# Optimization experiments

Measured on AMD Instinct MI355X. Metric: run time of the kernel, lower is better.

The kernel has to match this reference:

```python
import jax, jax.numpy as jnp
import numpy as np

N, QLEN, KLEN = 4, 2048, 2048
QDIM = KVDIM = 512
EMBED, HEADS = 1024, 16
HEAD_DIM = EMBED // HEADS


def setup_inputs() -> dict:
    key = jax.random.key(0)
    ks = jax.random.split(key, 7)
    return {
        "queries": jax.random.normal(ks[0], (N, QLEN, QDIM), dtype=jnp.float32),
        "keys": jax.random.normal(ks[1], (1, KLEN, KVDIM), dtype=jnp.float32),
        "values": jax.random.normal(ks[2], (1, KLEN, KVDIM), dtype=jnp.float32),
        "mask": jax.random.randint(ks[3], (N, 1, 1, KLEN), 0, 2, dtype=jnp.int32),
        "Wq": jax.random.normal(ks[4], (QDIM, EMBED), dtype=jnp.float32) * (QDIM ** -0.5),
        "Wk": jax.random.normal(ks[5], (KVDIM, EMBED), dtype=jnp.float32) * (KVDIM ** -0.5),
        "Wv": jax.random.normal(ks[6], (KVDIM, EMBED), dtype=jnp.float32) * (KVDIM ** -0.5),
    }


def reference(queries, keys, values, mask, Wq, Wk, Wv):
    # Projections (Linear, no bias)
    q = (queries @ Wq).reshape(N, QLEN, HEADS, HEAD_DIM)      # [N, Q, H, D]
    k = (keys @ Wk).reshape(KLEN, HEADS, HEAD_DIM)            # [K, H, D] (batch-1, shared)
    v = (values @ Wv).reshape(KLEN, HEADS, HEAD_DIM)          # [K, H, D]

    # energy: [N, H, Q, K]
    energy = jnp.einsum('nqhd,khd->nhqk', q, k)
    energy = jnp.where(mask == 0, jnp.float32(-1e20), energy)
    attn = jax.nn.softmax(energy / jnp.float32(HEAD_DIM ** 0.5), axis=3)

    out = jnp.einsum('nhqk,khd->nqhd', attn, v)               # [N, Q, H, D]
    return out.reshape(N, QLEN, EMBED)
```

## Files before the change

kernel.cpp:

```cpp
#include <hip/hip_runtime.h>

#define NB 4
#define QLEN 2048
#define KLEN 2048
#define QDIM 512
#define EMBED 1024
#define HEADS 16
#define HD 64

typedef __bf16 bf16x8 __attribute__((ext_vector_type(8)));
typedef float f32x2 __attribute__((ext_vector_type(2)));
typedef float f32x4 __attribute__((ext_vector_type(4)));
typedef float f32x16 __attribute__((ext_vector_type(16)));

#define CLOG 0.18033688011112042f

__device__ __forceinline__ float fexp2(float x) {
#if __has_builtin(__builtin_amdgcn_exp2f)
    return __builtin_amdgcn_exp2f(x);
#else
    float r;
    asm("v_exp_f32 %0, %1\n\ts_nop 1" : "=v"(r) : "v"(x));
    return r;
#endif
}

#if __has_builtin(__builtin_amdgcn_sched_barrier)
#define SCHED_FENCE() __builtin_amdgcn_sched_barrier(0)
#else
#define SCHED_FENCE()
#endif

__device__ __forceinline__ void dma16(const void* g, void* l) {
    __builtin_amdgcn_global_load_lds(
        (const __attribute__((address_space(1))) void*)g,
        (__attribute__((address_space(3))) void*)l, 16, 0, 0);
}

__global__ __launch_bounds__(256) void prep(const float* __restrict__ q,
                                            const float* __restrict__ k,
                                            const float* __restrict__ v,
                                            const float* __restrict__ Wq,
                                            const float* __restrict__ Wk,
                                            const float* __restrict__ Wv,
                                            __bf16* __restrict__ qd,
                                            __bf16* __restrict__ kd,
                                            __bf16* __restrict__ vd,
                                            __bf16* __restrict__ WtQ,
                                            __bf16* __restrict__ WtK,
                                            __bf16* __restrict__ WtV) {
    __shared__ float tile[32][33];
    int b = blockIdx.x, tid = threadIdx.x;
    if (b < 3072) {
        const float* src; __bf16* dst; int cb;
        if (b < 2048)      { src = q; dst = qd; cb = b; }
        else if (b < 2560) { src = k; dst = kd; cb = b - 2048; }
        else               { src = v; dst = vd; cb = b - 2560; }
        int i = (cb * 256 + tid) * 8;
        float4 a0 = *(const float4*)&src[i];
        float4 a1 = *(const float4*)&src[i + 4];
        bf16x8 o;
        o[0] = (__bf16)a0.x; o[1] = (__bf16)a0.y; o[2] = (__bf16)a0.z; o[3] = (__bf16)a0.w;
        o[4] = (__bf16)a1.x; o[5] = (__bf16)a1.y; o[6] = (__bf16)a1.z; o[7] = (__bf16)a1.w;
        *(bf16x8*)&dst[i] = o;
    } else {
        int tb = b - 3072;
        int which = tb >> 9, r = tb & 511;
        const float* src = (which == 0) ? Wq : (which == 1) ? Wk : Wv;
        __bf16* dst = (which == 0) ? WtQ : (which == 1) ? WtK : WtV;
        float scale = (which == 0) ? CLOG : 1.0f;
        int e0 = (r & 31) * 32, c0 = (r >> 5) * 32;
        int tx = tid & 31, ty = tid >> 5;
        for (int i = 0; i < 4; i++)
            tile[ty + 8 * i][tx] = src[(c0 + ty + 8 * i) * EMBED + e0 + tx];
        __syncthreads();
        for (int i = 0; i < 4; i++)
            dst[(e0 + ty + 8 * i) * QDIM + c0 + tx] = (__bf16)(tile[tx][ty + 8 * i] * scale);
    }
}

__device__ __forceinline__ void gemm_compute(const __bf16* As, const __bf16* Bs,
                                             int wr, int wc, int r16, int qq,
                                             f32x4 (&acc)[4][4]) {
    bf16x8 af[4], bq[4];
#pragma unroll
    for (int i = 0; i < 4; i++)
        af[i] = *(const bf16x8*)&As[(wr * 64 + i * 16 + r16) * 32 + qq * 8];
#pragma unroll
    for (int j = 0; j < 4; j++)
        bq[j] = *(const bf16x8*)&Bs[(wc * 64 + j * 16 + r16) * 32 + qq * 8];
#pragma unroll
    for (int i = 0; i < 4; i++)
#pragma unroll
        for (int j = 0; j < 4; j++)
            acc[i][j] = __builtin_amdgcn_mfma_f32_16x16x32_bf16(af[i], bq[j], acc[i][j], 0, 0, 0);
}

__device__ __forceinline__ void gemm128(const __bf16* __restrict__ A,
                                        const __bf16* __restrict__ Bt,
                                        __bf16* As0, __bf16* As1,
                                        __bf16* Bs0, __bf16* Bs1,
                                        int row0, int col0, f32x4 (&acc)[4][4]) {
    int tid = threadIdx.x, wave = tid >> 6, lane = tid & 63;
    int r16 = lane & 15, qq = lane >> 4;
    int wr = wave >> 1, wc = wave & 1;
    const __bf16* agp1 = A + (size_t)(row0 + (tid >> 2)) * QDIM + (tid & 3) * 8;
    const __bf16* agp2 = A + (size_t)(row0 + 64 + (tid >> 2)) * QDIM + (tid & 3) * 8;
    const __bf16* bgp1 = Bt + (size_t)(col0 + (tid >> 2)) * QDIM + (tid & 3) * 8;
    const __bf16* bgp2 = Bt + (size_t)(col0 + 64 + (tid >> 2)) * QDIM + (tid & 3) * 8;
    __bf16 *a0a = &As0[wave * 512], *a0b = &As0[2048 + wave * 512];
    __bf16 *a1a = &As1[wave * 512], *a1b = &As1[2048 + wave * 512];
    __bf16 *b0a = &Bs0[wave * 512], *b0b = &Bs0[2048 + wave * 512];
    __bf16 *b1a = &Bs1[wave * 512], *b1b = &Bs1[2048 + wave * 512];

    dma16(agp1, a0a); dma16(agp2, a0b);
    dma16(bgp1, b0a); dma16(bgp2, b0b);
    agp1 += 32; agp2 += 32; bgp1 += 32; bgp2 += 32;
    __syncthreads();

    for (int t = 0; t < 16; t += 2) {
        dma16(agp1, a1a); dma16(agp2, a1b);
        dma16(bgp1, b1a); dma16(bgp2, b1b);
        agp1 += 32; agp2 += 32; bgp1 += 32; bgp2 += 32;
        SCHED_FENCE();
        gemm_compute(As0, Bs0, wr, wc, r16, qq, acc);
        __syncthreads();
        if (t + 2 < 16) {
            dma16(agp1, a0a); dma16(agp2, a0b);
            dma16(bgp1, b0a); dma16(bgp2, b0b);
            agp1 += 32; agp2 += 32; bgp1 += 32; bgp2 += 32;
        }
        SCHED_FENCE();
        gemm_compute(As1, Bs1, wr, wc, r16, qq, acc);
        __syncthreads();
    }
}

__global__ __launch_bounds__(256) void proj_all(const __bf16* __restrict__ qin,
                                                const __bf16* __restrict__ kin,
                                                const __bf16* __restrict__ vin,
                                                const __bf16* __restrict__ wtq,
                                                const __bf16* __restrict__ wtk,
                                                const __bf16* __restrict__ wtv,
                                                __bf16* __restrict__ qout,
                                                __bf16* __restrict__ kout,
                                                __bf16* __restrict__ vtout) {
    __shared__ __align__(16) __bf16 As[2][128 * 32];
    __shared__ __align__(16) __bf16 Bs[2][128 * 32];
    int bid = blockIdx.x;
    const __bf16 *A, *Bt;
    int mode, b;
    if (bid < 512)      { A = qin; Bt = wtq; mode = 0; b = bid; }
    else if (bid < 640) { A = kin; Bt = wtk; mode = 1; b = bid - 512; }
    else                { A = wtv; Bt = vin; mode = 2; b = bid - 640; }
    int row0, col0;
    if (mode == 2) { row0 = (b >> 4) * 128; col0 = (b & 15) * 128; }
    else           { row0 = (b >> 3) * 128; col0 = (b & 7) * 128; }
    f32x4 acc[4][4] = {};
    gemm128(A, Bt, As[0], As[1], Bs[0], Bs[1], row0, col0, acc);
    int lane = threadIdx.x & 63, wave = threadIdx.x >> 6;
    int r16 = lane & 15, qq = lane >> 4;
    int wr = wave >> 1, wc = wave & 1;
#pragma unroll
    for (int i = 0; i < 4; i++)
#pragma unroll
        for (int j = 0; j < 4; j++)
#pragma unroll
            for (int rr = 0; rr < 4; rr++) {
                int grow = row0 + wr * 64 + i * 16 + qq * 4 + rr;
                int gcol = col0 + wc * 64 + j * 16 + r16;
                __bf16 v = (__bf16)acc[i][j][rr];
                if (mode == 0) {
                    int hh = gcol >> 6, d = gcol & 63;
                    int n = grow >> 11, qr = grow & 2047;
                    qout[((size_t)(n * HEADS + hh) * QLEN + qr) * HD + d] = v;
                } else if (mode == 1) {
                    int hh = gcol >> 6, d = gcol & 63;
                    kout[((size_t)hh * KLEN + grow) * HD + d] = v;
                } else {
                    vtout[(size_t)grow * KLEN + gcol] = v;
                }
            }
}

__device__ __forceinline__ void attn_tile(const __bf16* ksb, const __bf16* vsb,
                                          const float* mrow, const bf16x8 (&qfrag)[4],
                                          int col, int h,
                                          f32x16& o0, f32x16& o1, f32x2& rsl) {
    bf16x8 pfrag[4];
#pragma unroll
    for (int kt2 = 0; kt2 < 2; kt2++) {
        int R = kt2 * 32 + col;
        union { f32x16 v; f32x4 q[4]; } su;
#pragma unroll
        for (int G = 0; G < 4; G++)
            su.q[G] = *(const f32x4*)&mrow[kt2 * 32 + 16 * (G >> 1) + 8 * h + 4 * (G & 1)];
        f32x16 s = su.v;
        __builtin_amdgcn_s_setprio(1);
#pragma unroll
        for (int c = 0; c < 4; c++) {
            int cc = (2 * c + h) ^ (R & 7);
            bf16x8 kf = *(const bf16x8*)&ksb[(R * 8 + cc) * 8];
            s = __builtin_amdgcn_mfma_f32_32x32x16_bf16(kf, qfrag[c], s, 0, 0, 0);
        }
        __builtin_amdgcn_s_setprio(0);
#pragma unroll
        for (int G = 0; G < 4; G++) {
            int ci = 2 * kt2 + (G >> 1), e0 = (G & 1) * 4;
#pragma unroll
            for (int rr = 0; rr < 4; rr += 2) {
                float p0 = fexp2(s[4 * G + rr]);
                float p1 = fexp2(s[4 * G + rr + 1]);
                f32x2 pp; pp[0] = p0; pp[1] = p1;
                rsl += pp;
                pfrag[ci][e0 + rr] = (__bf16)p0;
                pfrag[ci][e0 + rr + 1] = (__bf16)p1;
            }
        }
    }
    __builtin_amdgcn_s_setprio(1);
#pragma unroll
    for (int c = 0; c < 4; c++) {
        int cc = (2 * c + h) ^ (col & 7);
        bf16x8 v0 = *(const bf16x8*)&vsb[(col * 8 + cc) * 8];
        bf16x8 v1 = *(const bf16x8*)&vsb[((32 + col) * 8 + cc) * 8];
        o0 = __builtin_amdgcn_mfma_f32_32x32x16_bf16(v0, pfrag[c], o0, 0, 0, 0);
        o1 = __builtin_amdgcn_mfma_f32_32x32x16_bf16(v1, pfrag[c], o1, 0, 0, 0);
    }
    __builtin_amdgcn_s_setprio(0);
}

__global__ __launch_bounds__(256, 4) void attn_kernel(const __bf16* __restrict__ qb,
                                                      const __bf16* __restrict__ kb,
                                                      const __bf16* __restrict__ vtb,
                                                      const int* __restrict__ mask,
                                                      float* __restrict__ out) {
    __shared__ __align__(16) __bf16 ks[2][4096];
    __shared__ __align__(16) __bf16 vs[2][4096];
    __shared__ __align__(16) float msf[KLEN];

    int tid = threadIdx.x, wave = tid >> 6, lane = tid & 63;
    int col = lane & 31, h = lane >> 5;
    int q0 = blockIdx.x * 128, hh = blockIdx.y, n = blockIdx.z;
    const __bf16* qg = qb + ((size_t)(n * HEADS + hh) * QLEN + q0 + wave * 32 + col) * HD;
    const __bf16* kg = kb + (size_t)hh * KLEN * HD;
    const __bf16* vg = vtb + (size_t)hh * HD * KLEN;
    const int* mg = mask + n * KLEN;

    bf16x8 qfrag[4];
#pragma unroll
    for (int c = 0; c < 4; c++) qfrag[c] = *(const bf16x8*)&qg[c * 16 + h * 8];

    int s1 = tid, R1 = s1 >> 3, c1 = (s1 & 7) ^ (R1 & 7);
    int s2 = tid + 256, R2 = s2 >> 3, c2 = (s2 & 7) ^ (R2 & 7);
    int g1 = (R1 & 0x33) | ((R1 & 4) << 1) | ((R1 & 8) >> 1);
    int g2 = (R2 & 0x33) | ((R2 & 4) << 1) | ((R2 & 8) >> 1);
    const __bf16* kgp1 = kg + g1 * HD + c1 * 8;
    const __bf16* kgp2 = kg + g2 * HD + c2 * 8;
    const __bf16* vgp1 = vg + (size_t)R1 * KLEN + c1 * 8;
    const __bf16* vgp2 = vg + (size_t)R2 * KLEN + c2 * 8;
    __bf16 *kl0a = &ks[0][wave * 512], *kl0b = &ks[0][2048 + wave * 512];
    __bf16 *kl1a = &ks[1][wave * 512], *kl1b = &ks[1][2048 + wave * 512];
    __bf16 *vl0a = &vs[0][wave * 512], *vl0b = &vs[0][2048 + wave * 512];
    __bf16 *vl1a = &vs[1][wave * 512], *vl1b = &vs[1][2048 + wave * 512];

    dma16(kgp1, kl0a); dma16(kgp2, kl0b);
    dma16(vgp1, vl0a); dma16(vgp2, vl0b);
    kgp1 += 64 * HD; kgp2 += 64 * HD; vgp1 += 64; vgp2 += 64;
    {
        int i8 = tid * 8;
        int4 ma = *(const int4*)&mg[i8];
        int4 mb = *(const int4*)&mg[i8 + 4];
        f32x4 fa, fb;
        fa[0] = ma.x ? 0.f : -1e30f; fa[1] = ma.y ? 0.f : -1e30f;
        fa[2] = ma.z ? 0.f : -1e30f; fa[3] = ma.w ? 0.f : -1e30f;
        fb[0] = mb.x ? 0.f : -1e30f; fb[1] = mb.y ? 0.f : -1e30f;
        fb[2] = mb.z ? 0.f : -1e30f; fb[3] = mb.w ? 0.f : -1e30f;
        *(f32x4*)&msf[i8] = fa;
        *(f32x4*)&msf[i8 + 4] = fb;
    }
    __syncthreads();

    f32x16 o0 = {}, o1 = {};
    f32x2 rsl = {};

    for (int t = 0; t < 32; t += 2) {
        dma16(kgp1, kl1a); dma16(kgp2, kl1b);
        dma16(vgp1, vl1a); dma16(vgp2, vl1b);
        kgp1 += 64 * HD; kgp2 += 64 * HD; vgp1 += 64; vgp2 += 64;
        SCHED_FENCE();
        attn_tile(ks[0], vs[0], &msf[t * 64], qfrag, col, h, o0, o1, rsl);
        __syncthreads();
        if (t + 2 < 32) {
            dma16(kgp1, kl0a); dma16(kgp2, kl0b);
            dma16(vgp1, vl0a); dma16(vgp2, vl0b);
            kgp1 += 64 * HD; kgp2 += 64 * HD; vgp1 += 64; vgp2 += 64;
        }
        SCHED_FENCE();
        attn_tile(ks[1], vs[1], &msf[(t + 1) * 64], qfrag, col, h, o0, o1, rsl);
        __syncthreads();
    }

    float rs = rsl[0] + rsl[1];
    rs += __shfl_xor(rs, 32);
    float inv = 1.0f / rs;
    float* op = out + ((size_t)n * QLEN + q0 + wave * 32 + col) * EMBED + hh * HD;
#pragma unroll
    for (int G = 0; G < 4; G++) {
        float4 t0, t1;
        t0.x = o0[4 * G + 0] * inv; t0.y = o0[4 * G + 1] * inv;
        t0.z = o0[4 * G + 2] * inv; t0.w = o0[4 * G + 3] * inv;
        t1.x = o1[4 * G + 0] * inv; t1.y = o1[4 * G + 1] * inv;
        t1.z = o1[4 * G + 2] * inv; t1.w = o1[4 * G + 3] * inv;
        *(float4*)&op[8 * G + 4 * h] = t0;
        *(float4*)&op[32 + 8 * G + 4 * h] = t1;
    }
}

extern "C" void kernel_launch(void* const* d_in, const int* in_sizes, int n_in,
                              void* d_out, int out_size, void* d_ws, size_t ws_size,
                              hipStream_t stream) {
    const float* queries = (const float*)d_in[0];
    const float* keys    = (const float*)d_in[1];
    const float* values  = (const float*)d_in[2];
    const int*   mask    = (const int*)d_in[3];
    const float* Wq      = (const float*)d_in[4];
    const float* Wk      = (const float*)d_in[5];
    const float* Wv      = (const float*)d_in[6];
    float* out = (float*)d_out;

    const size_t MiB = 1048576;
    char* ws = (char*)d_ws;
    __bf16* qbf   = (__bf16*)(ws);
    __bf16* kbf   = (__bf16*)(ws + 16 * MiB);
    __bf16* vtbf  = (__bf16*)(ws + 20 * MiB);
    __bf16* wtq   = (__bf16*)(ws + 24 * MiB);
    __bf16* wtk   = (__bf16*)(ws + 25 * MiB);
    __bf16* wtv   = (__bf16*)(ws + 26 * MiB);
    __bf16* qin   = (__bf16*)(ws + 27 * MiB);
    __bf16* kin   = (__bf16*)(ws + 35 * MiB);
    __bf16* vin   = (__bf16*)(ws + 37 * MiB);

    prep<<<4608, 256, 0, stream>>>(queries, keys, values, Wq, Wk, Wv,
                                   qin, kin, vin, wtq, wtk, wtv);
    proj_all<<<768, 256, 0, stream>>>(qin, kin, vin, wtq, wtk, wtv, qbf, kbf, vtbf);
    attn_kernel<<<dim3(QLEN / 128, HEADS, NB), 256, 0, stream>>>(qbf, kbf, vtbf, mask, out);
}
```

Baseline: 184.1 us.

## Read K/V tiles directly from global memory instead of LDS double-buffering

Removes the shared-memory staging of K and V tiles (async DMA into double-buffered LDS with swizzle and per-tile barriers). Each wave now loads its MFMA fragments straight from global memory, relying on L1/L2 caching since all waves of a block read the same K/V data. This drops the barriers and LDS traffic, and cuts LDS use, which can raise occupancy. The cost is redundant global/cache loads per wave and load latency that is no longer hidden by prefetch, leaving the MFMAs exposed to memory stalls.

```diff
diff --git a/kernel.cpp b/kernel.cpp
--- a/kernel.cpp
+++ b/kernel.cpp
@@ -183,14 +183,14 @@
             }
 }
 
-__device__ __forceinline__ void attn_tile(const __bf16* ksb, const __bf16* vsb,
+__device__ __forceinline__ void attn_tile(const __bf16* kt, const __bf16* vt,
                                           const float* mrow, const bf16x8 (&qfrag)[4],
-                                          int col, int h,
+                                          int col, int colp, int h,
                                           f32x16& o0, f32x16& o1, f32x2& rsl) {
     bf16x8 pfrag[4];
 #pragma unroll
     for (int kt2 = 0; kt2 < 2; kt2++) {
-        int R = kt2 * 32 + col;
+        const __bf16* kr = kt + (kt2 * 32 + colp) * HD + h * 8;
         union { f32x16 v; f32x4 q[4]; } su;
 #pragma unroll
         for (int G = 0; G < 4; G++)
@@ -199,8 +199,7 @@
         __builtin_amdgcn_s_setprio(1);
 #pragma unroll
         for (int c = 0; c < 4; c++) {
-            int cc = (2 * c + h) ^ (R & 7);
-            bf16x8 kf = *(const bf16x8*)&ksb[(R * 8 + cc) * 8];
+            bf16x8 kf = *(const bf16x8*)&kr[c * 16];
             s = __builtin_amdgcn_mfma_f32_32x32x16_bf16(kf, qfrag[c], s, 0, 0, 0);
         }
         __builtin_amdgcn_s_setprio(0);
@@ -218,12 +217,13 @@
             }
         }
     }
+    const __bf16* vr0 = vt + (size_t)col * KLEN + h * 8;
+    const __bf16* vr1 = vt + (size_t)(32 + col) * KLEN + h * 8;
     __builtin_amdgcn_s_setprio(1);
 #pragma unroll
     for (int c = 0; c < 4; c++) {
-        int cc = (2 * c + h) ^ (col & 7);
-        bf16x8 v0 = *(const bf16x8*)&vsb[(col * 8 + cc) * 8];
-        bf16x8 v1 = *(const bf16x8*)&vsb[((32 + col) * 8 + cc) * 8];
+        bf16x8 v0 = *(const bf16x8*)&vr0[c * 16];
+        bf16x8 v1 = *(const bf16x8*)&vr1[c * 16];
         o0 = __builtin_amdgcn_mfma_f32_32x32x16_bf16(v0, pfrag[c], o0, 0, 0, 0);
         o1 = __builtin_amdgcn_mfma_f32_32x32x16_bf16(v1, pfrag[c], o1, 0, 0, 0);
     }
@@ -235,12 +235,11 @@
                                                       const __bf16* __restrict__ vtb,
                                                       const int* __restrict__ mask,
                                                       float* __restrict__ out) {
-    __shared__ __align__(16) __bf16 ks[2][4096];
-    __shared__ __align__(16) __bf16 vs[2][4096];
     __shared__ __align__(16) float msf[KLEN];
 
     int tid = threadIdx.x, wave = tid >> 6, lane = tid & 63;
     int col = lane & 31, h = lane >> 5;
+    int colp = (col & 0x33) | ((col & 4) << 1) | ((col & 8) >> 1);
     int q0 = blockIdx.x * 128, hh = blockIdx.y, n = blockIdx.z;
     const __bf16* qg = qb + ((size_t)(n * HEADS + hh) * QLEN + q0 + wave * 32 + col) * HD;
     const __bf16* kg = kb + (size_t)hh * KLEN * HD;
@@ -251,22 +250,6 @@
 #pragma unroll
     for (int c = 0; c < 4; c++) qfrag[c] = *(const bf16x8*)&qg[c * 16 + h * 8];
 
-    int s1 = tid, R1 = s1 >> 3, c1 = (s1 & 7) ^ (R1 & 7);
-    int s2 = tid + 256, R2 = s2 >> 3, c2 = (s2 & 7) ^ (R2 & 7);
-    int g1 = (R1 & 0x33) | ((R1 & 4) << 1) | ((R1 & 8) >> 1);
-    int g2 = (R2 & 0x33) | ((R2 & 4) << 1) | ((R2 & 8) >> 1);
-    const __bf16* kgp1 = kg + g1 * HD + c1 * 8;
-    const __bf16* kgp2 = kg + g2 * HD + c2 * 8;
-    const __bf16* vgp1 = vg + (size_t)R1 * KLEN + c1 * 8;
-    const __bf16* vgp2 = vg + (size_t)R2 * KLEN + c2 * 8;
-    __bf16 *kl0a = &ks[0][wave * 512], *kl0b = &ks[0][2048 + wave * 512];
-    __bf16 *kl1a = &ks[1][wave * 512], *kl1b = &ks[1][2048 + wave * 512];
-    __bf16 *vl0a = &vs[0][wave * 512], *vl0b = &vs[0][2048 + wave * 512];
-    __bf16 *vl1a = &vs[1][wave * 512], *vl1b = &vs[1][2048 + wave * 512];
-
-    dma16(kgp1, kl0a); dma16(kgp2, kl0b);
-    dma16(vgp1, vl0a); dma16(vgp2, vl0b);
-    kgp1 += 64 * HD; kgp2 += 64 * HD; vgp1 += 64; vgp2 += 64;
     {
         int i8 = tid * 8;
         int4 ma = *(const int4*)&mg[i8];
@@ -284,22 +267,9 @@
     f32x16 o0 = {}, o1 = {};
     f32x2 rsl = {};
 
-    for (int t = 0; t < 32; t += 2) {
-        dma16(kgp1, kl1a); dma16(kgp2, kl1b);
-        dma16(vgp1, vl1a); dma16(vgp2, vl1b);
-        kgp1 += 64 * HD; kgp2 += 64 * HD; vgp1 += 64; vgp2 += 64;
-        SCHED_FENCE();
-        attn_tile(ks[0], vs[0], &msf[t * 64], qfrag, col, h, o0, o1, rsl);
-        __syncthreads();
-        if (t + 2 < 32) {
-            dma16(kgp1, kl0a); dma16(kgp2, kl0b);
-            dma16(vgp1, vl0a); dma16(vgp2, vl0b);
-            kgp1 += 64 * HD; kgp2 += 64 * HD; vgp1 += 64; vgp2 += 64;
-        }
-        SCHED_FENCE();
-        attn_tile(ks[1], vs[1], &msf[(t + 1) * 64], qfrag, col, h, o0, o1, rsl);
-        __syncthreads();
-    }
+    for (int t = 0; t < 32; ++t)
+        attn_tile(kg + (size_t)t * 64 * HD, vg + t * 64, &msf[t * 64],
+                  qfrag, col, colp, h, o0, o1, rsl);
 
     float rs = rsl[0] + rsl[1];
     rs += __shfl_xor(rs, 32);
```

New measurement: 344.2 us. +87.0%, slower.

## Double attention block to 8 waves covering 256 queries sharing K/V tiles

Applied to the files above, without the earlier changes.

The attention kernel now launches 512 threads per block, each block handling 256 query rows instead of 128, and half as many blocks. Each thread issues one K and one V async copy per tile rather than two, so every K/V tile loaded into shared memory serves twice as many waves. This halves global K/V traffic and per-thread load work, at the cost of larger blocks, fewer blocks in the grid (512), and more waves stalling at each block-wide barrier.

```diff
diff --git a/kernel.cpp b/kernel.cpp
--- a/kernel.cpp
+++ b/kernel.cpp
@@ -230,7 +230,7 @@
     __builtin_amdgcn_s_setprio(0);
 }
 
-__global__ __launch_bounds__(256, 4) void attn_kernel(const __bf16* __restrict__ qb,
+__global__ __launch_bounds__(512, 4) void attn_kernel(const __bf16* __restrict__ qb,
                                                       const __bf16* __restrict__ kb,
                                                       const __bf16* __restrict__ vtb,
                                                       const int* __restrict__ mask,
@@ -241,7 +241,7 @@
 
     int tid = threadIdx.x, wave = tid >> 6, lane = tid & 63;
     int col = lane & 31, h = lane >> 5;
-    int q0 = blockIdx.x * 128, hh = blockIdx.y, n = blockIdx.z;
+    int q0 = blockIdx.x * 256, hh = blockIdx.y, n = blockIdx.z;
     const __bf16* qg = qb + ((size_t)(n * HEADS + hh) * QLEN + q0 + wave * 32 + col) * HD;
     const __bf16* kg = kb + (size_t)hh * KLEN * HD;
     const __bf16* vg = vtb + (size_t)hh * HD * KLEN;
@@ -251,33 +251,22 @@
 #pragma unroll
     for (int c = 0; c < 4; c++) qfrag[c] = *(const bf16x8*)&qg[c * 16 + h * 8];
 
-    int s1 = tid, R1 = s1 >> 3, c1 = (s1 & 7) ^ (R1 & 7);
-    int s2 = tid + 256, R2 = s2 >> 3, c2 = (s2 & 7) ^ (R2 & 7);
+    int R1 = tid >> 3, c1 = (tid & 7) ^ (R1 & 7);
     int g1 = (R1 & 0x33) | ((R1 & 4) << 1) | ((R1 & 8) >> 1);
-    int g2 = (R2 & 0x33) | ((R2 & 4) << 1) | ((R2 & 8) >> 1);
     const __bf16* kgp1 = kg + g1 * HD + c1 * 8;
-    const __bf16* kgp2 = kg + g2 * HD + c2 * 8;
     const __bf16* vgp1 = vg + (size_t)R1 * KLEN + c1 * 8;
-    const __bf16* vgp2 = vg + (size_t)R2 * KLEN + c2 * 8;
-    __bf16 *kl0a = &ks[0][wave * 512], *kl0b = &ks[0][2048 + wave * 512];
-    __bf16 *kl1a = &ks[1][wave * 512], *kl1b = &ks[1][2048 + wave * 512];
-    __bf16 *vl0a = &vs[0][wave * 512], *vl0b = &vs[0][2048 + wave * 512];
-    __bf16 *vl1a = &vs[1][wave * 512], *vl1b = &vs[1][2048 + wave * 512];
-
-    dma16(kgp1, kl0a); dma16(kgp2, kl0b);
-    dma16(vgp1, vl0a); dma16(vgp2, vl0b);
-    kgp1 += 64 * HD; kgp2 += 64 * HD; vgp1 += 64; vgp2 += 64;
+    __bf16 *kl0 = &ks[0][wave * 512], *kl1 = &ks[1][wave * 512];
+    __bf16 *vl0 = &vs[0][wave * 512], *vl1 = &vs[1][wave * 512];
+
+    dma16(kgp1, kl0); dma16(vgp1, vl0);
+    kgp1 += 64 * HD; vgp1 += 64;
     {
-        int i8 = tid * 8;
-        int4 ma = *(const int4*)&mg[i8];
-        int4 mb = *(const int4*)&mg[i8 + 4];
-        f32x4 fa, fb;
+        int i4 = tid * 4;
+        int4 ma = *(const int4*)&mg[i4];
+        f32x4 fa;
         fa[0] = ma.x ? 0.f : -1e30f; fa[1] = ma.y ? 0.f : -1e30f;
         fa[2] = ma.z ? 0.f : -1e30f; fa[3] = ma.w ? 0.f : -1e30f;
-        fb[0] = mb.x ? 0.f : -1e30f; fb[1] = mb.y ? 0.f : -1e30f;
-        fb[2] = mb.z ? 0.f : -1e30f; fb[3] = mb.w ? 0.f : -1e30f;
-        *(f32x4*)&msf[i8] = fa;
-        *(f32x4*)&msf[i8 + 4] = fb;
+        *(f32x4*)&msf[i4] = fa;
     }
     __syncthreads();
 
@@ -285,16 +274,14 @@
     f32x2 rsl = {};
 
     for (int t = 0; t < 32; t += 2) {
-        dma16(kgp1, kl1a); dma16(kgp2, kl1b);
-        dma16(vgp1, vl1a); dma16(vgp2, vl1b);
-        kgp1 += 64 * HD; kgp2 += 64 * HD; vgp1 += 64; vgp2 += 64;
+        dma16(kgp1, kl1); dma16(vgp1, vl1);
+        kgp1 += 64 * HD; vgp1 += 64;
         SCHED_FENCE();
         attn_tile(ks[0], vs[0], &msf[t * 64], qfrag, col, h, o0, o1, rsl);
         __syncthreads();
         if (t + 2 < 32) {
-            dma16(kgp1, kl0a); dma16(kgp2, kl0b);
-            dma16(vgp1, vl0a); dma16(vgp2, vl0b);
-            kgp1 += 64 * HD; kgp2 += 64 * HD; vgp1 += 64; vgp2 += 64;
+            dma16(kgp1, kl0); dma16(vgp1, vl0);
+            kgp1 += 64 * HD; vgp1 += 64;
         }
         SCHED_FENCE();
         attn_tile(ks[1], vs[1], &msf[(t + 1) * 64], qfrag, col, h, o0, o1, rsl);
@@ -344,5 +331,5 @@
     prep<<<4608, 256, 0, stream>>>(queries, keys, values, Wq, Wk, Wv,
                                    qin, kin, vin, wtq, wtk, wtv);
     proj_all<<<768, 256, 0, stream>>>(qin, kin, vin, wtq, wtk, wtv, qbf, kbf, vtbf);
-    attn_kernel<<<dim3(QLEN / 128, HEADS, NB), 256, 0, stream>>>(qbf, kbf, vtbf, mask, out);
-}
+    attn_kernel<<<dim3(QLEN / 256, HEADS, NB), 512, 0, stream>>>(qbf, kbf, vtbf, mask, out);
+}
```

Result: no change. 181.5 us (-1.4%).

## Process two 32-row query tiles per wave to reuse K/V LDS loads

Applied to the files above, without the earlier changes.

Each wave now handles 64 query rows (two 32-row sub-tiles) instead of 32, so each block covers 256 queries and the grid halves. K and V fragments read from shared memory are reused across both sub-tiles, halving LDS traffic and global K/V streaming per query. The cost is roughly doubled accumulator and fragment registers, reflected in lowering launch bounds occupancy from 4 to 2 blocks per CU, and fewer blocks in the grid (512).

```diff
diff --git a/kernel.cpp b/kernel.cpp
--- a/kernel.cpp
+++ b/kernel.cpp
@@ -183,11 +183,14 @@
             }
 }
 
-__device__ __forceinline__ void attn_tile(const __bf16* ksb, const __bf16* vsb,
-                                          const float* mrow, const bf16x8 (&qfrag)[4],
-                                          int col, int h,
-                                          f32x16& o0, f32x16& o1, f32x2& rsl) {
-    bf16x8 pfrag[4];
+__device__ __forceinline__ void attn_tile2(const __bf16* ksb, const __bf16* vsb,
+                                           const float* mrow,
+                                           const bf16x8 (&qfA)[4], const bf16x8 (&qfB)[4],
+                                           int col, int h,
+                                           f32x16& oA0, f32x16& oA1,
+                                           f32x16& oB0, f32x16& oB1,
+                                           f32x2& rslA, f32x2& rslB) {
+    bf16x8 pfA[4], pfB[4];
 #pragma unroll
     for (int kt2 = 0; kt2 < 2; kt2++) {
         int R = kt2 * 32 + col;
@@ -195,13 +198,19 @@
 #pragma unroll
         for (int G = 0; G < 4; G++)
             su.q[G] = *(const f32x4*)&mrow[kt2 * 32 + 16 * (G >> 1) + 8 * h + 4 * (G & 1)];
-        f32x16 s = su.v;
+        f32x16 sA, sB;
         __builtin_amdgcn_s_setprio(1);
 #pragma unroll
         for (int c = 0; c < 4; c++) {
             int cc = (2 * c + h) ^ (R & 7);
             bf16x8 kf = *(const bf16x8*)&ksb[(R * 8 + cc) * 8];
-            s = __builtin_amdgcn_mfma_f32_32x32x16_bf16(kf, qfrag[c], s, 0, 0, 0);
+            if (c == 0) {
+                sA = __builtin_amdgcn_mfma_f32_32x32x16_bf16(kf, qfA[0], su.v, 0, 0, 0);
+                sB = __builtin_amdgcn_mfma_f32_32x32x16_bf16(kf, qfB[0], su.v, 0, 0, 0);
+            } else {
+                sA = __builtin_amdgcn_mfma_f32_32x32x16_bf16(kf, qfA[c], sA, 0, 0, 0);
+                sB = __builtin_amdgcn_mfma_f32_32x32x16_bf16(kf, qfB[c], sB, 0, 0, 0);
+            }
         }
         __builtin_amdgcn_s_setprio(0);
 #pragma unroll
@@ -209,12 +218,18 @@
             int ci = 2 * kt2 + (G >> 1), e0 = (G & 1) * 4;
 #pragma unroll
             for (int rr = 0; rr < 4; rr += 2) {
-                float p0 = fexp2(s[4 * G + rr]);
-                float p1 = fexp2(s[4 * G + rr + 1]);
-                f32x2 pp; pp[0] = p0; pp[1] = p1;
-                rsl += pp;
-                pfrag[ci][e0 + rr] = (__bf16)p0;
-                pfrag[ci][e0 + rr + 1] = (__bf16)p1;
+                float a0 = fexp2(sA[4 * G + rr]);
+                float a1 = fexp2(sA[4 * G + rr + 1]);
+                float b0 = fexp2(sB[4 * G + rr]);
+                float b1 = fexp2(sB[4 * G + rr + 1]);
+                f32x2 pa; pa[0] = a0; pa[1] = a1;
+                f32x2 pb; pb[0] = b0; pb[1] = b1;
+                rslA += pa;
+                rslB += pb;
+                pfA[ci][e0 + rr] = (__bf16)a0;
+                pfA[ci][e0 + rr + 1] = (__bf16)a1;
+                pfB[ci][e0 + rr] = (__bf16)b0;
+                pfB[ci][e0 + rr + 1] = (__bf16)b1;
             }
         }
     }
@@ -224,13 +239,15 @@
         int cc = (2 * c + h) ^ (col & 7);
         bf16x8 v0 = *(const bf16x8*)&vsb[(col * 8 + cc) * 8];
         bf16x8 v1 = *(const bf16x8*)&vsb[((32 + col) * 8 + cc) * 8];
-        o0 = __builtin_amdgcn_mfma_f32_32x32x16_bf16(v0, pfrag[c], o0, 0, 0, 0);
-        o1 = __builtin_amdgcn_mfma_f32_32x32x16_bf16(v1, pfrag[c], o1, 0, 0, 0);
+        oA0 = __builtin_amdgcn_mfma_f32_32x32x16_bf16(v0, pfA[c], oA0, 0, 0, 0);
+        oA1 = __builtin_amdgcn_mfma_f32_32x32x16_bf16(v1, pfA[c], oA1, 0, 0, 0);
+        oB0 = __builtin_amdgcn_mfma_f32_32x32x16_bf16(v0, pfB[c], oB0, 0, 0, 0);
+        oB1 = __builtin_amdgcn_mfma_f32_32x32x16_bf16(v1, pfB[c], oB1, 0, 0, 0);
     }
     __builtin_amdgcn_s_setprio(0);
 }
 
-__global__ __launch_bounds__(256, 4) void attn_kernel(const __bf16* __restrict__ qb,
+__global__ __launch_bounds__(256, 2) void attn_kernel(const __bf16* __restrict__ qb,
                                                       const __bf16* __restrict__ kb,
                                                       const __bf16* __restrict__ vtb,
                                                       const int* __restrict__ mask,
@@ -241,15 +258,19 @@
 
     int tid = threadIdx.x, wave = tid >> 6, lane = tid & 63;
     int col = lane & 31, h = lane >> 5;
-    int q0 = blockIdx.x * 128, hh = blockIdx.y, n = blockIdx.z;
-    const __bf16* qg = qb + ((size_t)(n * HEADS + hh) * QLEN + q0 + wave * 32 + col) * HD;
+    int q0 = blockIdx.x * 256, hh = blockIdx.y, n = blockIdx.z;
+    const __bf16* qgA = qb + ((size_t)(n * HEADS + hh) * QLEN + q0 + wave * 64 + col) * HD;
+    const __bf16* qgB = qgA + 32 * HD;
     const __bf16* kg = kb + (size_t)hh * KLEN * HD;
     const __bf16* vg = vtb + (size_t)hh * HD * KLEN;
     const int* mg = mask + n * KLEN;
 
-    bf16x8 qfrag[4];
-#pragma unroll
-    for (int c = 0; c < 4; c++) qfrag[c] = *(const bf16x8*)&qg[c * 16 + h * 8];
+    bf16x8 qfA[4], qfB[4];
+#pragma unroll
+    for (int c = 0; c < 4; c++) {
+        qfA[c] = *(const bf16x8*)&qgA[c * 16 + h * 8];
+        qfB[c] = *(const bf16x8*)&qgB[c * 16 + h * 8];
+    }
 
     int s1 = tid, R1 = s1 >> 3, c1 = (s1 & 7) ^ (R1 & 7);
     int s2 = tid + 256, R2 = s2 >> 3, c2 = (s2 & 7) ^ (R2 & 7);
@@ -281,15 +302,16 @@
     }
     __syncthreads();
 
-    f32x16 o0 = {}, o1 = {};
-    f32x2 rsl = {};
+    f32x16 oA0 = {}, oA1 = {}, oB0 = {}, oB1 = {};
+    f32x2 rslA = {}, rslB = {};
 
     for (int t = 0; t < 32; t += 2) {
         dma16(kgp1, kl1a); dma16(kgp2, kl1b);
         dma16(vgp1, vl1a); dma16(vgp2, vl1b);
         kgp1 += 64 * HD; kgp2 += 64 * HD; vgp1 += 64; vgp2 += 64;
         SCHED_FENCE();
-        attn_tile(ks[0], vs[0], &msf[t * 64], qfrag, col, h, o0, o1, rsl);
+        attn_tile2(ks[0], vs[0], &msf[t * 64], qfA, qfB, col, h,
+                   oA0, oA1, oB0, oB1, rslA, rslB);
         __syncthreads();
         if (t + 2 < 32) {
             dma16(kgp1, kl0a); dma16(kgp2, kl0b);
@@ -297,23 +319,34 @@
             kgp1 += 64 * HD; kgp2 += 64 * HD; vgp1 += 64; vgp2 += 64;
         }
         SCHED_FENCE();
-        attn_tile(ks[1], vs[1], &msf[(t + 1) * 64], qfrag, col, h, o0, o1, rsl);
-        __syncthreads();
-    }
-
-    float rs = rsl[0] + rsl[1];
-    rs += __shfl_xor(rs, 32);
-    float inv = 1.0f / rs;
-    float* op = out + ((size_t)n * QLEN + q0 + wave * 32 + col) * EMBED + hh * HD;
+        attn_tile2(ks[1], vs[1], &msf[(t + 1) * 64], qfA, qfB, col, h,
+                   oA0, oA1, oB0, oB1, rslA, rslB);
+        __syncthreads();
+    }
+
+    float rsA = rslA[0] + rslA[1];
+    float rsB = rslB[0] + rslB[1];
+    rsA += __shfl_xor(rsA, 32);
+    rsB += __shfl_xor(rsB, 32);
+    float invA = 1.0f / rsA;
+    float invB = 1.0f / rsB;
+    float* opA = out + ((size_t)n * QLEN + q0 + wave * 64 + col) * EMBED + hh * HD;
+    float* opB = opA + (size_t)32 * EMBED;
 #pragma unroll
     for (int G = 0; G < 4; G++) {
         float4 t0, t1;
-        t0.x = o0[4 * G + 0] * inv; t0.y = o0[4 * G + 1] * inv;
-        t0.z = o0[4 * G + 2] * inv; t0.w = o0[4 * G + 3] * inv;
-        t1.x = o1[4 * G + 0] * inv; t1.y = o1[4 * G + 1] * inv;
-        t1.z = o1[4 * G + 2] * inv; t1.w = o1[4 * G + 3] * inv;
-        *(float4*)&op[8 * G + 4 * h] = t0;
-        *(float4*)&op[32 + 8 * G + 4 * h] = t1;
+        t0.x = oA0[4 * G + 0] * invA; t0.y = oA0[4 * G + 1] * invA;
+        t0.z = oA0[4 * G + 2] * invA; t0.w = oA0[4 * G + 3] * invA;
+        t1.x = oA1[4 * G + 0] * invA; t1.y = oA1[4 * G + 1] * invA;
+        t1.z = oA1[4 * G + 2] * invA; t1.w = oA1[4 * G + 3] * invA;
+        *(float4*)&opA[8 * G + 4 * h] = t0;
+        *(float4*)&opA[32 + 8 * G + 4 * h] = t1;
+        t0.x = oB0[4 * G + 0] * invB; t0.y = oB0[4 * G + 1] * invB;
+        t0.z = oB0[4 * G + 2] * invB; t0.w = oB0[4 * G + 3] * invB;
+        t1.x = oB1[4 * G + 0] * invB; t1.y = oB1[4 * G + 1] * invB;
+        t1.z = oB1[4 * G + 2] * invB; t1.w = oB1[4 * G + 3] * invB;
+        *(float4*)&opB[8 * G + 4 * h] = t0;
+        *(float4*)&opB[32 + 8 * G + 4 * h] = t1;
     }
 }
 
@@ -344,5 +377,5 @@
     prep<<<4608, 256, 0, stream>>>(queries, keys, values, Wq, Wk, Wv,
                                    qin, kin, vin, wtq, wtk, wtv);
     proj_all<<<768, 256, 0, stream>>>(qin, kin, vin, wtq, wtk, wtv, qbf, kbf, vtbf);
-    attn_kernel<<<dim3(QLEN / 128, HEADS, NB), 256, 0, stream>>>(qbf, kbf, vtbf, mask, out);
-}
+    attn_kernel<<<dim3(QLEN / 256, HEADS, NB), 256, 0, stream>>>(qbf, kbf, vtbf, mask, out);
+}
```

New measurement: 182.8 us. About the same (-0.7%).
